# Kernel optimization log

Hardware: AMD Instinct MI355X
Metric: run time of the kernel (lower is better)

The kernel has to match this reference:

```python
import jax, jax.numpy as jnp
import numpy as np

N, C, H, W = 32, 128, 96, 96
K = 64  # num_clusters
EPS = 1e-12

def _l2norm(v, axis):
    # matches torch F.normalize: v / max(||v||, eps)
    n = jnp.sqrt(jnp.sum(v * v, axis=axis, keepdims=True))
    return v / jnp.maximum(n, EPS)

def setup_inputs() -> dict:
    key = jax.random.key(0)
    ks = jax.random.split(key, 5)
    return {
        "x": jax.random.normal(ks[0], (N, C, H, W), dtype=jnp.float32),
        "conv_w": jax.random.normal(ks[1], (K, C), dtype=jnp.float32) * 0.1,
        "centroids": jax.random.uniform(ks[2], (K, C), dtype=jnp.float32),
        "proj_w": jax.random.normal(ks[3], (C, K * C), dtype=jnp.float32) * 0.02,
        "proj_b": jax.random.normal(ks[4], (C,), dtype=jnp.float32) * 0.01,
    }

def reference(x, conv_w, centroids, proj_w, proj_b):
    n, c = x.shape[:2]
    x = _l2norm(x, axis=1)                       # normalize_input over channels
    xf = x.reshape(n, c, -1)                     # [N, C, HW]
    # 1x1 conv == per-pixel matmul: [N, K, HW]
    logits = jnp.einsum('kc,nch->nkh', conv_w, xf)
    soft = jax.nn.softmax(logits, axis=1)        # softmax over clusters
    # fused VLAD: sum_h a_{nkh} (x_{nch} - c_{kc})
    vlad = jnp.einsum('nkh,nch->nkc', soft, xf) \
         - soft.sum(axis=-1)[:, :, None] * centroids[None]
    vlad = _l2norm(vlad, axis=2)                 # intra-normalization
    vlad = vlad.reshape(n, -1)                   # [N, K*C]
    vlad = _l2norm(vlad, axis=1)
    return vlad @ proj_w.T + proj_b              # [N, C]
```

## Files before the change

kernel.cpp:

```cpp
#include <hip/hip_runtime.h>
#include <hip/hip_bf16.h>

typedef float f32x16 __attribute__((ext_vector_type(16)));
typedef short short8 __attribute__((ext_vector_type(8)));

#define N_IMG 32
#define C_CH  128
#define HW    9216
#define K_CL  64
#define EPSF  1e-12f

#define BPI   16
#define PPB   576
#define NHALF 9

#define WS_VLAD 0
#define WS_ASUM (N_IMG*K_CL*C_CH)
#define WS_ZERO (WS_ASUM + N_IMG*K_CL)
#define WS_PART WS_ZERO
#define NPART   (N_IMG*BPI)
#define WS_ASP  (WS_PART + NPART*K_CL*C_CH/2)
#define WS_STORE_TOT (WS_ASP + NPART*K_CL)

__device__ __forceinline__ unsigned short bfb(float f) {
    __hip_bfloat16 h = __float2bfloat16(f);
    return *reinterpret_cast<unsigned short*>(&h);
}
__device__ __forceinline__ float b2f(unsigned short s) {
    return __uint_as_float(((unsigned)s) << 16);
}

typedef const __attribute__((address_space(1))) void gv_t;
typedef __attribute__((address_space(3))) void lv_t;
__device__ __forceinline__ void gload16(const void* g, void* l) {
    __builtin_amdgcn_global_load_lds((gv_t*)g, (lv_t*)l, 16, 0, 0);
}
#define SBAR()  __builtin_amdgcn_s_barrier()
#define WAITL() do { asm volatile("s_waitcnt lgkmcnt(0)" ::: "memory"); \
                     __builtin_amdgcn_sched_barrier(0); } while (0)
#define WAITV() do { asm volatile("s_waitcnt vmcnt(0)" ::: "memory"); \
                     __builtin_amdgcn_sched_barrier(0); } while (0)

__global__ void k_zero(float* __restrict__ p, int cnt) {
    int i = blockIdx.x * blockDim.x + threadIdx.x;
    if (i < cnt) p[i] = 0.f;
}

__global__ __launch_bounds__(256, 2) void k_fused10(
    const float* __restrict__ x, const float* __restrict__ conv_w,
    float* __restrict__ vlad, float* __restrict__ asum,
    unsigned short* __restrict__ part, float* __restrict__ aspart, int use_part)
{
    __shared__ __align__(16) char cw_lds[64 * 256];
    __shared__ __align__(16) char xs_lds[128 * 256];
    __shared__ __align__(16) char s_lds [64 * 128];
    __shared__ __align__(16) char x_lds [128 * 128];
    __shared__ __align__(16) float smpart[2][64];
    __shared__ __align__(16) float invt[64];

    const int t  = threadIdx.x;
    const int w  = t >> 6;
    const int l  = t & 63;
    const int lp = l & 31;
    const int h  = l >> 5;
    const int n    = blockIdx.x / BPI;
    const int pblk = (blockIdx.x % BPI) * PPB;

    #pragma unroll
    for (int r = 0; r < 16; ++r) {
        int e  = t + 256 * r;
        int k  = e >> 6;
        int c2 = (e & 63) << 1;
        unsigned pa = (unsigned)bfb(conv_w[k * C_CH + c2]) |
                      ((unsigned)bfb(conv_w[k * C_CH + c2 + 1]) << 16);
        int addr = (((k << 8) | (c2 << 1)) ^ ((k & 7) << 4));
        *reinterpret_cast<unsigned*>(cw_lds + addr) = pa;
    }

    f32x16 va0, va1;
    #pragma unroll
    for (int r = 0; r < 16; ++r) { va0[r] = 0.f; va1[r] = 0.f; }
    float asum_acc = 0.f;

    const int kh  = w >> 1;
    const int p   = ((w & 1) << 5) + lp;
    const int p2  = p << 1;
    const int ks  = t >> 2;
    const int st4 = t & 3;
    const float* xbase = x + (size_t)n * C_CH * HW;

    const int pxo   = (l & 15) << 2;
    const int crow0 = (w << 5) + (l >> 4);

    const int swzL = (lp & 7) << 4;
    const int hx   = h << 4;
    const int bCW  = (((kh << 5) + lp) << 8) | (hx ^ swzL);
    const int bXS  = (p << 2) + (h << 11);
    const int cB   = (w << 5) + lp;
    const int bXf  = (cB << 7) | (hx ^ swzL);
    const int bS0  = (lp << 7)        | (hx ^ swzL);
    const int bS1  = ((32 + lp) << 7) | (hx ^ swzL);
    int baseS[4];
    #pragma unroll
    for (int j = 0; j < 4; ++j)
        baseS[j] = (kh << 12) + (h << 9) + (p2 ^ (j << 4) ^ (h << 6));

    {
        const float* src0 = xbase + pblk + pxo;
        #pragma unroll
        for (int j = 0; j < 8; ++j)
            gload16(src0 + (size_t)(crow0 + 4 * j) * HW,
                    xs_lds + (((w << 5) + 4 * j) << 8));
    }
    WAITL(); WAITV(); SBAR();

    for (int it = 0; it < NHALF; ++it) {
        if (it > 0) { WAITV(); SBAR(); }

        float ss = 0.f;
        short8 xb[8];
        #pragma unroll
        for (int s8 = 0; s8 < 8; ++s8) {
            #pragma unroll
            for (int i = 0; i < 8; ++i) {
                float f = *reinterpret_cast<const float*>(
                    xs_lds + bXS + ((16 * s8 + i) << 8));
                ss += f * f;
                xb[s8][i] = (short)bfb(f);
            }
        }
        ss += __shfl_xor(ss, 32);
        const float scn = 1.f / fmaxf(sqrtf(ss), EPSF);

        WAITL(); SBAR();

        if (it + 1 < NHALF) {
            const float* src0 = xbase + pblk + (it + 1) * 64 + pxo;
            #pragma unroll
            for (int j = 0; j < 8; ++j)
                gload16(src0 + (size_t)(crow0 + 4 * j) * HW,
                        xs_lds + (((w << 5) + 4 * j) << 8));
        }

        f32x16 d;
        #pragma unroll
        for (int r = 0; r < 16; ++r) d[r] = 0.f;
        #pragma unroll
        for (int s8 = 0; s8 < 8; ++s8) {
            short8 a = *reinterpret_cast<const short8*>(cw_lds + (bCW ^ (s8 << 5)));
            d = __builtin_amdgcn_mfma_f32_32x32x16_bf16(a, xb[s8], d, 0, 0, 0);
        }

        float e[16];
        float sm = 0.f;
        #pragma unroll
        for (int r = 0; r < 16; ++r) { e[r] = __expf(d[r] * scn); sm += e[r]; }
        sm += __shfl_xor(sm, 32);
        if (h == 0) smpart[kh][p] = sm;
        WAITL(); SBAR();

        const float inv = 1.f / (smpart[0][p] + smpart[1][p]);
        const float sc2 = scn * inv;

        #pragma unroll
        for (int r = 0; r < 16; ++r) {
            const int imm = ((r & 3) << 7) + ((r >> 2) << 10);
            *reinterpret_cast<short*>(s_lds + (baseS[r & 3] + imm)) = (short)bfb(e[r]);
        }
        if (kh == 0) {
            #pragma unroll
            for (int j = 0; j < 8; ++j) {
                const int bx_ = (p2 ^ (j << 4)) + (h << 10);
                #pragma unroll
                for (int s = 0; s < 8; ++s)
                    *reinterpret_cast<short*>(x_lds + (bx_ + ((16 * s + j) << 7))) =
                        (short)bfb(b2f((unsigned short)xb[s][j]) * sc2);
            }
            if (h == 0) invt[p] = inv;
        }
        WAITL(); SBAR();

        #pragma unroll
        for (int sp = 0; sp < 4; ++sp) {
            short8 bf = *reinterpret_cast<const short8*>(x_lds + (bXf ^ (sp << 5)));
            short8 s0 = *reinterpret_cast<const short8*>(s_lds + (bS0 ^ (sp << 5)));
            short8 s1 = *reinterpret_cast<const short8*>(s_lds + (bS1 ^ (sp << 5)));
            va0 = __builtin_amdgcn_mfma_f32_32x32x16_bf16(s0, bf, va0, 0, 0, 0);
            va1 = __builtin_amdgcn_mfma_f32_32x32x16_bf16(s1, bf, va1, 0, 0, 0);
        }

        {
            const int rowb = ks << 7;
            const int swz  = (ks & 7) << 4;
            const float* ivp = invt + (st4 << 4);
            float a = 0.f;
            #pragma unroll
            for (int g = 0; g < 2; ++g) {
                int off = (st4 << 5) | (g << 4);
                short8 u = *reinterpret_cast<const short8*>(s_lds + (rowb | (off ^ swz)));
                float4 ia = *reinterpret_cast<const float4*>(ivp + g * 8);
                float4 ib = *reinterpret_cast<const float4*>(ivp + g * 8 + 4);
                a += b2f((unsigned short)u[0]) * ia.x + b2f((unsigned short)u[1]) * ia.y +
                     b2f((unsigned short)u[2]) * ia.z + b2f((unsigned short)u[3]) * ia.w;
                a += b2f((unsigned short)u[4]) * ib.x + b2f((unsigned short)u[5]) * ib.y +
                     b2f((unsigned short)u[6]) * ib.z + b2f((unsigned short)u[7]) * ib.w;
            }
            asum_acc += a;
        }
    }

    if (use_part) {
        unsigned short* pb_ = part + (size_t)blockIdx.x * (K_CL * C_CH) + cB;
        #pragma unroll
        for (int r = 0; r < 16; ++r) {
            const int kr = (r & 3) + 8 * (r >> 2) + 4 * h;
            pb_[(kr)      * C_CH] = bfb(va0[r]);
            pb_[(32 + kr) * C_CH] = bfb(va1[r]);
        }
        float vv = asum_acc;
        vv += __shfl_xor(vv, 1);
        vv += __shfl_xor(vv, 2);
        if (st4 == 0) aspart[blockIdx.x * K_CL + ks] = vv;
    } else {
        float* vb = vlad + (size_t)n * K_CL * C_CH;
        #pragma unroll
        for (int r = 0; r < 16; ++r) {
            const int kr = (r & 3) + 8 * (r >> 2) + 4 * h;
            atomicAdd(vb + (kr)      * C_CH + cB, va0[r]);
            atomicAdd(vb + (32 + kr) * C_CH + cB, va1[r]);
        }
        float vv = asum_acc;
        vv += __shfl_xor(vv, 1);
        vv += __shfl_xor(vv, 2);
        if (st4 == 0) atomicAdd(asum + n * K_CL + ks, vv);
    }
}

__global__ void k_rows_part(float* __restrict__ vlad, const unsigned short* __restrict__ part,
                            const float* __restrict__ aspart,
                            const float* __restrict__ cent)
{
    const int bx = blockIdx.x;
    const int n = bx >> 6, k = bx & 63;
    const int c = threadIdx.x;
    const int b0 = n * BPI;
    float v = 0.f, a = 0.f;
    #pragma unroll
    for (int b = 0; b < BPI; ++b) {
        v += b2f(part[(size_t)(b0 + b) * (K_CL * C_CH) + k * C_CH + c]);
        a += aspart[(b0 + b) * K_CL + k];
    }
    v -= a * cent[k * C_CH + c];
    float ssq = v * v;
    #pragma unroll
    for (int m = 32; m >= 1; m >>= 1) ssq += __shfl_xor(ssq, m);
    __shared__ float sb[2];
    if ((threadIdx.x & 63) == 0) sb[threadIdx.x >> 6] = ssq;
    __syncthreads();
    float tot = sb[0] + sb[1];
    float sc = 1.f / fmaxf(sqrtf(tot), EPSF);
    vlad[((size_t)n * K_CL + k) * C_CH + c] = v * sc;
}

__global__ void k_rows(float* __restrict__ vlad, const float* __restrict__ asum,
                       const float* __restrict__ cent)
{
    const int bx = blockIdx.x;
    const int n = bx >> 6, k = bx & 63;
    const int c = threadIdx.x;
    float a = asum[n * K_CL + k];
    size_t idx = ((size_t)n * K_CL + k) * C_CH + c;
    float v = vlad[idx] - a * cent[k * C_CH + c];
    float ssq = v * v;
    #pragma unroll
    for (int m = 32; m >= 1; m >>= 1) ssq += __shfl_xor(ssq, m);
    __shared__ float sb[2];
    if ((threadIdx.x & 63) == 0) sb[threadIdx.x >> 6] = ssq;
    __syncthreads();
    float tot = sb[0] + sb[1];
    float sc = 1.f / fmaxf(sqrtf(tot), EPSF);
    vlad[idx] = v * sc;
}

__global__ __launch_bounds__(256) void k_proj3(
    const float* __restrict__ vlad, const float* __restrict__ pw,
    const float* __restrict__ pbias, float* __restrict__ out)
{
    const int j  = blockIdx.x;
    const int n0 = blockIdx.y << 2;
    const int t  = threadIdx.x;
    const float4* wp = (const float4*)(pw + (size_t)j * (K_CL * C_CH));
    float4 wr[8];
    #pragma unroll
    for (int r = 0; r < 8; ++r) wr[r] = wp[t + 256 * r];
    __shared__ float sb[4], sb2[4];
    const float bias = pbias[j];
    #pragma unroll
    for (int u = 0; u < 4; ++u) {
        const int n = n0 + u;
        const float4* vp = (const float4*)(vlad + (size_t)n * (K_CL * C_CH));
        float s = 0.f, nn = 0.f;
        #pragma unroll
        for (int r = 0; r < 8; ++r) {
            float4 a = vp[t + 256 * r];
            s  += a.x * wr[r].x + a.y * wr[r].y + a.z * wr[r].z + a.w * wr[r].w;
            nn += a.x * a.x + a.y * a.y + a.z * a.z + a.w * a.w;
        }
        #pragma unroll
        for (int m = 32; m >= 1; m >>= 1) {
            s  += __shfl_xor(s, m);
            nn += __shfl_xor(nn, m);
        }
        if ((t & 63) == 0) { sb[t >> 6] = s; sb2[t >> 6] = nn; }
        __syncthreads();
        if (t == 0) {
            float tot = sb[0] + sb[1] + sb[2] + sb[3];
            float tss = sb2[0] + sb2[1] + sb2[2] + sb2[3];
            float inv = 1.f / fmaxf(sqrtf(tss), EPSF);
            out[n * C_CH + j] = tot * inv + bias;
        }
        __syncthreads();
    }
}

extern "C" void kernel_launch(void* const* d_in, const int* in_sizes, int n_in,
                              void* d_out, int out_size, void* d_ws, size_t ws_size,
                              hipStream_t stream)
{
    const float* x      = (const float*)d_in[0];
    const float* conv_w = (const float*)d_in[1];
    const float* cent   = (const float*)d_in[2];
    const float* pw     = (const float*)d_in[3];
    const float* pbias  = (const float*)d_in[4];
    float* out = (float*)d_out;
    float* ws  = (float*)d_ws;

    float* vlad            = ws + WS_VLAD;
    float* asum            = ws + WS_ASUM;
    unsigned short* part   = (unsigned short*)(ws + WS_PART);
    float* aspart          = ws + WS_ASP;

    const int use_part = (ws_size >= (size_t)WS_STORE_TOT * sizeof(float)) ? 1 : 0;

    if (!use_part) {
        hipLaunchKernelGGL(k_zero, dim3((WS_ZERO + 255) / 256), dim3(256), 0, stream,
                           ws, WS_ZERO);
    }
    hipLaunchKernelGGL(k_fused10, dim3(N_IMG * BPI), dim3(256), 0, stream,
                       x, conv_w, vlad, asum, part, aspart, use_part);
    if (use_part) {
        hipLaunchKernelGGL(k_rows_part, dim3(N_IMG * K_CL), dim3(C_CH), 0, stream,
                           vlad, part, aspart, cent);
    } else {
        hipLaunchKernelGGL(k_rows, dim3(N_IMG * K_CL), dim3(C_CH), 0, stream,
                           vlad, asum, cent);
    }
    hipLaunchKernelGGL(k_proj3, dim3(C_CH, N_IMG / 4), dim3(256), 0, stream,
                       vlad, pw, pbias, out);
}
```

Measured before the change: 57.96 us.

## Read x twice: direct global loads for logits, swizzled LDS DMA for aggregation

The per-pixel x values for the norm and logit MFMA are now read straight from global memory, not from the LDS staging buffer. The DMA'd LDS copy, now XOR-swizzled, feeds the aggregation MFMA directly. This removes the separate scaled bf16 x_lds buffer and its scattered stores by applying the scn*inv scale on the fly from a small per-pixel table. The initial DMA is issued before the conv_w conversion so the two overlap. The cost is that x is fetched from global memory twice (relying on cache hits), and the next DMA is issued later in each iteration, which shortens the window for overlapping it with compute.

```diff
diff --git a/kernel.cpp b/kernel.cpp
--- a/kernel.cpp
+++ b/kernel.cpp
@@ -36,17 +36,16 @@
     __builtin_amdgcn_global_load_lds((gv_t*)g, (lv_t*)l, 16, 0, 0);
 }
 #define SBAR()  __builtin_amdgcn_s_barrier()
-#define WAITL() do { asm volatile("s_waitcnt lgkmcnt(0)" ::: "memory"); \
-                     __builtin_amdgcn_sched_barrier(0); } while (0)
-#define WAITV() do { asm volatile("s_waitcnt vmcnt(0)" ::: "memory"); \
-                     __builtin_amdgcn_sched_barrier(0); } while (0)
+#define SCHED() __builtin_amdgcn_sched_barrier(0)
+#define WAITL() do { asm volatile("s_waitcnt lgkmcnt(0)" ::: "memory"); SCHED(); } while (0)
+#define WAITV() do { asm volatile("s_waitcnt vmcnt(0)" ::: "memory"); SCHED(); } while (0)
 
 __global__ void k_zero(float* __restrict__ p, int cnt) {
     int i = blockIdx.x * blockDim.x + threadIdx.x;
     if (i < cnt) p[i] = 0.f;
 }
 
-__global__ __launch_bounds__(256, 2) void k_fused10(
+__global__ __launch_bounds__(256, 2) void k_fused11(
     const float* __restrict__ x, const float* __restrict__ conv_w,
     float* __restrict__ vlad, float* __restrict__ asum,
     unsigned short* __restrict__ part, float* __restrict__ aspart, int use_part)
@@ -54,9 +53,9 @@
     __shared__ __align__(16) char cw_lds[64 * 256];
     __shared__ __align__(16) char xs_lds[128 * 256];
     __shared__ __align__(16) char s_lds [64 * 128];
-    __shared__ __align__(16) char x_lds [128 * 128];
     __shared__ __align__(16) float smpart[2][64];
     __shared__ __align__(16) float invt[64];
+    __shared__ __align__(16) float sc2t[64];
 
     const int t  = threadIdx.x;
     const int w  = t >> 6;
@@ -66,6 +65,36 @@
     const int n    = blockIdx.x / BPI;
     const int pblk = (blockIdx.x % BPI) * PPB;
 
+    const int kh  = w >> 1;
+    const int p   = ((w & 1) << 5) + lp;
+    const int p2  = p << 1;
+    const int ks  = t >> 2;
+    const int st4 = t & 3;
+    const float* xbase = x + (size_t)n * C_CH * HW;
+
+    const int swzL = (lp & 7) << 4;
+    const int hx   = h << 4;
+    const int bCW  = (((kh << 5) + lp) << 8) | (hx ^ swzL);
+    const int cB   = (w << 5) + lp;
+    const int swzC = (cB & 7) << 4;
+    const int bS0  = (lp << 7)        | (hx ^ swzL);
+    const int bS1  = ((32 + lp) << 7) | (hx ^ swzL);
+    int baseS[4];
+    #pragma unroll
+    for (int j = 0; j < 4; ++j)
+        baseS[j] = (kh << 12) + (h << 9) + (p2 ^ (j << 4) ^ (h << 6));
+
+    #define ISSUE_DMA(OFF) do { \
+        _Pragma("unroll") \
+        for (int j_ = 0; j_ < 8; ++j_) { \
+            const int rloc = (l >> 4) + 4 * j_; \
+            const int pxs  = ((l & 15) ^ (rloc & 7)) << 2; \
+            gload16(xbase + pblk + (OFF) + (size_t)((w << 5) + rloc) * HW + pxs, \
+                    xs_lds + ((((w << 5) + 4 * j_)) << 8)); \
+        } } while (0)
+
+    ISSUE_DMA(0);
+    SCHED();
     #pragma unroll
     for (int r = 0; r < 16; ++r) {
         int e  = t + 256 * r;
@@ -82,65 +111,27 @@
     for (int r = 0; r < 16; ++r) { va0[r] = 0.f; va1[r] = 0.f; }
     float asum_acc = 0.f;
 
-    const int kh  = w >> 1;
-    const int p   = ((w & 1) << 5) + lp;
-    const int p2  = p << 1;
-    const int ks  = t >> 2;
-    const int st4 = t & 3;
-    const float* xbase = x + (size_t)n * C_CH * HW;
-
-    const int pxo   = (l & 15) << 2;
-    const int crow0 = (w << 5) + (l >> 4);
-
-    const int swzL = (lp & 7) << 4;
-    const int hx   = h << 4;
-    const int bCW  = (((kh << 5) + lp) << 8) | (hx ^ swzL);
-    const int bXS  = (p << 2) + (h << 11);
-    const int cB   = (w << 5) + lp;
-    const int bXf  = (cB << 7) | (hx ^ swzL);
-    const int bS0  = (lp << 7)        | (hx ^ swzL);
-    const int bS1  = ((32 + lp) << 7) | (hx ^ swzL);
-    int baseS[4];
-    #pragma unroll
-    for (int j = 0; j < 4; ++j)
-        baseS[j] = (kh << 12) + (h << 9) + (p2 ^ (j << 4) ^ (h << 6));
-
-    {
-        const float* src0 = xbase + pblk + pxo;
-        #pragma unroll
-        for (int j = 0; j < 8; ++j)
-            gload16(src0 + (size_t)(crow0 + 4 * j) * HW,
-                    xs_lds + (((w << 5) + 4 * j) << 8));
-    }
-    WAITL(); WAITV(); SBAR();
+    WAITL(); SBAR();
 
     for (int it = 0; it < NHALF; ++it) {
-        if (it > 0) { WAITV(); SBAR(); }
-
+        if (it) { WAITL(); SBAR(); }
+
+        const float* xp = xbase + pblk + it * 64 + p;
         float ss = 0.f;
         short8 xb[8];
         #pragma unroll
-        for (int s8 = 0; s8 < 8; ++s8) {
+        for (int s = 0; s < 8; ++s) {
+            float xv[8];
             #pragma unroll
-            for (int i = 0; i < 8; ++i) {
-                float f = *reinterpret_cast<const float*>(
-                    xs_lds + bXS + ((16 * s8 + i) << 8));
-                ss += f * f;
-                xb[s8][i] = (short)bfb(f);
-            }
+            for (int i = 0; i < 8; ++i)
+                xv[i] = xp[(size_t)(16 * s + 8 * h + i) * HW];
+            #pragma unroll
+            for (int i = 0; i < 8; ++i) ss += xv[i] * xv[i];
+            #pragma unroll
+            for (int i = 0; i < 8; ++i) xb[s][i] = (short)bfb(xv[i]);
         }
         ss += __shfl_xor(ss, 32);
         const float scn = 1.f / fmaxf(sqrtf(ss), EPSF);
-
-        WAITL(); SBAR();
-
-        if (it + 1 < NHALF) {
-            const float* src0 = xbase + pblk + (it + 1) * 64 + pxo;
-            #pragma unroll
-            for (int j = 0; j < 8; ++j)
-                gload16(src0 + (size_t)(crow0 + 4 * j) * HW,
-                        xs_lds + (((w << 5) + 4 * j) << 8));
-        }
 
         f32x16 d;
         #pragma unroll
@@ -151,43 +142,47 @@
             d = __builtin_amdgcn_mfma_f32_32x32x16_bf16(a, xb[s8], d, 0, 0, 0);
         }
 
-        float e[16];
         float sm = 0.f;
         #pragma unroll
-        for (int r = 0; r < 16; ++r) { e[r] = __expf(d[r] * scn); sm += e[r]; }
+        for (int r = 0; r < 16; ++r) {
+            float e = __expf(d[r] * scn);
+            sm += e;
+            const int imm = ((r & 3) << 7) + ((r >> 2) << 10);
+            *reinterpret_cast<short*>(s_lds + (baseS[r & 3] + imm)) = (short)bfb(e);
+        }
         sm += __shfl_xor(sm, 32);
         if (h == 0) smpart[kh][p] = sm;
         WAITL(); SBAR();
 
         const float inv = 1.f / (smpart[0][p] + smpart[1][p]);
-        const float sc2 = scn * inv;
-
-        #pragma unroll
-        for (int r = 0; r < 16; ++r) {
-            const int imm = ((r & 3) << 7) + ((r >> 2) << 10);
-            *reinterpret_cast<short*>(s_lds + (baseS[r & 3] + imm)) = (short)bfb(e[r]);
-        }
-        if (kh == 0) {
-            #pragma unroll
-            for (int j = 0; j < 8; ++j) {
-                const int bx_ = (p2 ^ (j << 4)) + (h << 10);
-                #pragma unroll
-                for (int s = 0; s < 8; ++s)
-                    *reinterpret_cast<short*>(x_lds + (bx_ + ((16 * s + j) << 7))) =
-                        (short)bfb(b2f((unsigned short)xb[s][j]) * sc2);
-            }
-            if (h == 0) invt[p] = inv;
-        }
+        if (kh == 0 && h == 0) { invt[p] = inv; sc2t[p] = scn * inv; }
         WAITL(); SBAR();
 
+        WAITV();
+
         #pragma unroll
         for (int sp = 0; sp < 4; ++sp) {
-            short8 bf = *reinterpret_cast<const short8*>(x_lds + (bXf ^ (sp << 5)));
+            const int boffp = (sp << 6) + (h << 5);
+            const int a0 = (cB << 8) + (boffp ^ swzC);
+            float4 f0 = *reinterpret_cast<const float4*>(xs_lds + a0);
+            float4 f1 = *reinterpret_cast<const float4*>(xs_lds + (a0 ^ 16));
+            const int pix0 = (sp << 4) + (h << 3);
+            float4 s2a = *reinterpret_cast<const float4*>(sc2t + pix0);
+            float4 s2b = *reinterpret_cast<const float4*>(sc2t + pix0 + 4);
+            short8 bf;
+            bf[0] = (short)bfb(f0.x * s2a.x); bf[1] = (short)bfb(f0.y * s2a.y);
+            bf[2] = (short)bfb(f0.z * s2a.z); bf[3] = (short)bfb(f0.w * s2a.w);
+            bf[4] = (short)bfb(f1.x * s2b.x); bf[5] = (short)bfb(f1.y * s2b.y);
+            bf[6] = (short)bfb(f1.z * s2b.z); bf[7] = (short)bfb(f1.w * s2b.w);
             short8 s0 = *reinterpret_cast<const short8*>(s_lds + (bS0 ^ (sp << 5)));
             short8 s1 = *reinterpret_cast<const short8*>(s_lds + (bS1 ^ (sp << 5)));
             va0 = __builtin_amdgcn_mfma_f32_32x32x16_bf16(s0, bf, va0, 0, 0, 0);
             va1 = __builtin_amdgcn_mfma_f32_32x32x16_bf16(s1, bf, va1, 0, 0, 0);
         }
+
+        WAITL();
+        if (it + 1 < NHALF) ISSUE_DMA((it + 1) * 64);
+        SCHED();
 
         {
             const int rowb = ks << 7;
@@ -234,6 +229,7 @@
         vv += __shfl_xor(vv, 2);
         if (st4 == 0) atomicAdd(asum + n * K_CL + ks, vv);
     }
+    #undef ISSUE_DMA
 }
 
 __global__ void k_rows_part(float* __restrict__ vlad, const unsigned short* __restrict__ part,
@@ -346,7 +342,7 @@
         hipLaunchKernelGGL(k_zero, dim3((WS_ZERO + 255) / 256), dim3(256), 0, stream,
                            ws, WS_ZERO);
     }
-    hipLaunchKernelGGL(k_fused10, dim3(N_IMG * BPI), dim3(256), 0, stream,
+    hipLaunchKernelGGL(k_fused11, dim3(N_IMG * BPI), dim3(256), 0, stream,
                        x, conv_w, vlad, asum, part, aspart, use_part);
     if (use_part) {
         hipLaunchKernelGGL(k_rows_part, dim3(N_IMG * K_CL), dim3(C_CH), 0, stream,
```

Result: slower. 61.20 us (+5.6%).
